# Optimization experiments

Measured on AMD Instinct MI355X. Metric: run time of the kernel, lower is better.

## Reference

```python
import jax, jax.numpy as jnp
import numpy as np

EPS = 1e-5
K = 20

def knn_idx(x, k):
    # x: (B, N, C) -> indices of k nearest neighbors (by negative squared distance, includes self)
    sq = jnp.sum(x * x, axis=-1)                                  # (B, N)
    d = 2.0 * jnp.einsum('bnc,bmc->bnm', x, x) - sq[:, :, None] - sq[:, None, :]
    return jax.lax.top_k(d, k)[1]                                 # (B, N, k)

def edge_conv(x, k, W, g, b, rm, rv):
    # x: (B, N, C); W: (O, 2C); BN params: (O,). Returns (B, N, O).
    idx = knn_idx(x, k)
    feat = jax.vmap(lambda xt, i: xt[i])(x, idx)                  # (B, N, k, C) neighbor gather
    ctr = jnp.broadcast_to(x[:, :, None, :], feat.shape)
    edge = jnp.concatenate([feat - ctr, ctr], axis=-1)            # (B, N, k, 2C)
    h = jnp.einsum('bnkc,oc->bnko', edge, W)                      # 1x1 conv
    h = g * (h - rm) * jax.lax.rsqrt(rv + EPS) + b                # BN (eval, running stats)
    h = jnp.where(h > 0, h, 0.2 * h)                              # LeakyReLU(0.2)
    return jnp.max(h, axis=2)                                     # max over k

def bn(h, g, b, rm, rv):
    return g * (h - rm) * jax.lax.rsqrt(rv + EPS) + b

def lrelu(h):
    return jnp.where(h > 0, h, 0.2 * h)

def _bn_params(key, c):
    k1, k2 = jax.random.split(key)
    g = 1.0 + 0.1 * jax.random.normal(k1, (c,), dtype=jnp.float32)
    b = 0.1 * jax.random.normal(k2, (c,), dtype=jnp.float32)
    return g, b, jnp.zeros((c,), jnp.float32), jnp.ones((c,), jnp.float32)

def setup_inputs() -> dict:
    key = jax.random.key(0)
    ks = jax.random.split(key, 16)
    B, Cin, N = 8, 6, 4096
    d = {'x': jax.random.normal(ks[0], (B, Cin, N), dtype=jnp.float32)}
    def w(k, o, i):
        return jax.random.normal(k, (o, i), dtype=jnp.float32) * (1.0 / np.sqrt(i))
    d['W1'] = w(ks[1], 64, 12);   d['g1'], d['b1'], d['m1'], d['v1'] = _bn_params(ks[2], 64)
    d['W2'] = w(ks[3], 64, 128);  d['g2'], d['b2'], d['m2'], d['v2'] = _bn_params(ks[4], 64)
    d['W3'] = w(ks[5], 128, 128); d['g3'], d['b3'], d['m3'], d['v3'] = _bn_params(ks[6], 128)
    d['W4'] = w(ks[7], 256, 256); d['g4'], d['b4'], d['m4'], d['v4'] = _bn_params(ks[8], 256)
    d['W5'] = w(ks[9], 1024, 512); d['g5'], d['b5'], d['m5'], d['v5'] = _bn_params(ks[10], 1024)
    d['L1'] = w(ks[11], 512, 2048); d['gl1'], d['bl1'], d['ml1'], d['vl1'] = _bn_params(ks[12], 512)
    d['L2'] = w(ks[13], 256, 512); d['L2b'] = jnp.zeros((256,), jnp.float32)
    d['gl2'], d['bl2'], d['ml2'], d['vl2'] = _bn_params(ks[14], 256)
    d['L3'] = w(ks[15], 2, 256);  d['L3b'] = jnp.zeros((2,), jnp.float32)
    return d

def reference(x, W1, g1, b1, m1, v1, W2, g2, b2, m2, v2, W3, g3, b3, m3, v3,
              W4, g4, b4, m4, v4, W5, g5, b5, m5, v5,
              L1, gl1, bl1, ml1, vl1, L2, L2b, gl2, bl2, ml2, vl2, L3, L3b):
    xt = jnp.transpose(x, (0, 2, 1))                              # (B, N, 6)
    x1 = edge_conv(xt, K, W1, g1, b1, m1, v1)                     # (B, N, 64)
    x2 = edge_conv(x1, K, W2, g2, b2, m2, v2)                     # (B, N, 64)
    x3 = edge_conv(x2, K, W3, g3, b3, m3, v3)                     # (B, N, 128)
    x4 = edge_conv(x3, K, W4, g4, b4, m4, v4)                     # (B, N, 256)
    xc = jnp.concatenate([x1, x2, x3, x4], axis=-1)               # (B, N, 512)
    h = lrelu(bn(jnp.einsum('bnc,oc->bno', xc, W5), g5, b5, m5, v5))  # (B, N, 1024)
    pooled = jnp.concatenate([jnp.max(h, axis=1), jnp.mean(h, axis=1)], axis=-1)  # (B, 2048)
    o = lrelu(bn(pooled @ L1.T, gl1, bl1, ml1, vl1))
    o = lrelu(bn(o @ L2.T + L2b, gl2, bl2, ml2, vl2))
    return o @ L3.T + L3b                                         # (B, 2)
```

## Files before the change

kernel.cpp:

```cpp
#include <hip/hip_runtime.h>


#define NPTS   4096
#define NB     8
#define BNR    32768
#define KNN    20
#define EPSBN  1e-5f
#define CAP    12

__device__ __forceinline__ float lrelu(float x){ return x > 0.f ? x : 0.2f*x; }

__global__ __launch_bounds__(256) void k_transpose_pad(const float* __restrict__ x,
                                                       float* __restrict__ xt){
  int id = blockIdx.x*256 + threadIdx.x;
  int b = id >> 12, n = id & (NPTS-1);
  const float* xb = x + (size_t)b*6*NPTS + n;
  float* o = xt + (size_t)id*8;
#pragma unroll
  for (int c = 0; c < 6; ++c) o[c] = xb[(size_t)c*NPTS];
  o[6] = 0.f; o[7] = 0.f;
}

__global__ __launch_bounds__(256) void k_sqnorm(const float* __restrict__ X, int xstride, int c4,
                                                float* __restrict__ sq){
  int id = blockIdx.x*256 + threadIdx.x;
  const float4* r = (const float4*)(X + (size_t)id*xstride);
  float s = 0.f;
  for (int c = 0; c < c4; ++c){ float4 v = r[c]; s += v.x*v.x + v.y*v.y + v.z*v.z + v.w*v.w; }
  sq[id] = s;
}

template<int K>
__global__ __launch_bounds__(256) void k_knn_fused(const float* __restrict__ X, int xstride,
                                                   const float* __restrict__ sqv,
                                                   int* __restrict__ idx){
  constexpr int BK = (K < 32) ? K : 32;
  __shared__ float As[BK][68];
  __shared__ float Bs[BK][132];
  __shared__ float sqs[128];
  __shared__ float thr[64];
  __shared__ float lv[64][KNN];
  __shared__ int   li[64][KNN];
  __shared__ int   cnt[64];
  __shared__ float cv[64][CAP];
  __shared__ int   ci[64][CAP];

  const int b  = blockIdx.y;
  const int i0 = blockIdx.x * 64;
  const int tid = threadIdx.x, tx = tid & 15, ty = tid >> 4;
  const float* Xb  = X + (size_t)b * NPTS * xstride;
  const float* sqb = sqv + b * NPTS;

  if (tid < 64){
    thr[tid] = -3e38f; cnt[tid] = 0;
#pragma unroll
    for (int j = 0; j < KNN; ++j){ lv[tid][j] = -3e38f; li[tid][j] = 0; }
  }
  float sqi[4];
#pragma unroll
  for (int r = 0; r < 4; ++r) sqi[r] = sqb[i0 + ty*4 + r];

  for (int j0 = 0; j0 < NPTS; j0 += 128){
    float acc[4][8] = {};
    for (int k0 = 0; k0 < K; k0 += BK){
      {
        int row = tid & 63, q = tid >> 6;
        const float* src = Xb + (size_t)(i0 + row)*xstride + k0;
#pragma unroll
        for (int k = q*(BK/4); k < (q+1)*(BK/4); ++k) As[k][row] = src[k];
      }
      {
        int col = tid & 127, h = tid >> 7;
        const float* src = Xb + (size_t)(j0 + col)*xstride + k0;
#pragma unroll
        for (int k = h*(BK/2); k < (h+1)*(BK/2); ++k) Bs[k][col] = src[k];
      }
      if (k0 == 0 && tid < 128) sqs[tid] = sqb[j0 + tid];
      __syncthreads();
#pragma unroll
      for (int kk = 0; kk < BK; ++kk){
        float a[4], bb_[8];
        *(float4*)a        = *(const float4*)&As[kk][ty*4];
        *(float4*)&bb_[0]  = *(const float4*)&Bs[kk][tx*4];
        *(float4*)&bb_[4]  = *(const float4*)&Bs[kk][64 + tx*4];
#pragma unroll
        for (int r = 0; r < 4; ++r)
#pragma unroll
          for (int c = 0; c < 8; ++c)
            acc[r][c] = fmaf(a[r], bb_[c], acc[r][c]);
      }
      __syncthreads();
    }
    float sq8[8];
#pragma unroll
    for (int c = 0; c < 4; ++c){ sq8[c] = sqs[tx*4 + c]; sq8[c+4] = sqs[64 + tx*4 + c]; }

    unsigned pending = 0xFFFFFFFFu;
    while (true){
      if (pending){
        float tr[4];
#pragma unroll
        for (int r = 0; r < 4; ++r) tr[r] = thr[ty*4 + r];
#pragma unroll
        for (int r = 0; r < 4; ++r)
#pragma unroll
          for (int c = 0; c < 8; ++c){
            unsigned bit = 1u << (r*8 + c);
            if (pending & bit){
              float val = 2.f*acc[r][c] - sqi[r] - sq8[c];
              if (val <= tr[r]) pending &= ~bit;
              else {
                int row = ty*4 + r;
                int pos = atomicAdd(&cnt[row], 1);
                if (pos < CAP){
                  int col = (c < 4) ? (j0 + tx*4 + c) : (j0 + 64 + tx*4 + c - 4);
                  cv[row][pos] = val; ci[row][pos] = col;
                  pending &= ~bit;
                }
              }
            }
          }
      }
      int any = __syncthreads_or(pending != 0u);
      if (tid < 64){
        int n = min(cnt[tid], CAP);
        for (int i2 = 0; i2 < n; ++i2){
          float val = cv[tid][i2]; int cc = ci[tid][i2];
          if (val > lv[tid][KNN-1]){
            int j = KNN-1;
            while (j > 0 && lv[tid][j-1] < val){
              lv[tid][j] = lv[tid][j-1]; li[tid][j] = li[tid][j-1]; --j;
            }
            lv[tid][j] = val; li[tid][j] = cc;
          }
        }
        thr[tid] = lv[tid][KNN-1];
        cnt[tid] = 0;
      }
      __syncthreads();
      if (!any) break;
    }
  }
  if (tid < 64){
    int gn = b*NPTS + i0 + tid;
#pragma unroll
    for (int j = 0; j < KNN; ++j) idx[(size_t)gn*KNN + j] = li[tid][j];
  }
}

__global__ __launch_bounds__(256) void k_gemm_pq(const float* __restrict__ X, int xstride, int Kdim,
                                                 const float* __restrict__ W, int wstride, int Och,
                                                 float* __restrict__ PQ){
  __shared__ float Xs[16][132];
  __shared__ float Ws[16][68];
  const int m0 = blockIdx.x*128, o0 = blockIdx.y*64;
  const int tid = threadIdx.x, tx = tid & 15, ty = tid >> 4;
  const int O2 = 2*Och;
  float acc[8][4] = {};
  for (int k0 = 0; k0 < Kdim; k0 += 16){
#pragma unroll
    for (int i = 0; i < 8; ++i){
      int li = tid + 256*i;
      int row = li >> 4, kk = li & 15;
      bool ok = (k0 + kk) < Kdim;
      Xs[kk][row] = ok ? X[(size_t)(m0+row)*xstride + k0+kk] : 0.f;
    }
#pragma unroll
    for (int i = 0; i < 4; ++i){
      int li = tid + 256*i;
      int row = li >> 4, kk = li & 15;
      int orow = o0 + row;
      const float* wr = (orow < Och) ? (W + (size_t)orow*wstride)
                                     : (W + (size_t)(orow-Och)*wstride + Kdim);
      bool ok = (k0 + kk) < Kdim;
      Ws[kk][row] = ok ? wr[k0+kk] : 0.f;
    }
    __syncthreads();
#pragma unroll
    for (int kk = 0; kk < 16; ++kk){
      float xa[8], wb[4];
      *(float4*)&xa[0] = *(const float4*)&Xs[kk][ty*8];
      *(float4*)&xa[4] = *(const float4*)&Xs[kk][ty*8+4];
      *(float4*)wb     = *(const float4*)&Ws[kk][tx*4];
#pragma unroll
      for (int i = 0; i < 8; ++i)
#pragma unroll
        for (int j = 0; j < 4; ++j)
          acc[i][j] = fmaf(xa[i], wb[j], acc[i][j]);
    }
    __syncthreads();
  }
#pragma unroll
  for (int i = 0; i < 8; ++i){
    float4 v = make_float4(acc[i][0], acc[i][1], acc[i][2], acc[i][3]);
    *(float4*)&PQ[(size_t)(m0+ty*8+i)*O2 + o0 + tx*4] = v;
  }
}

__global__ __launch_bounds__(256) void k_gather_conv(const float* __restrict__ PQ,
                                                     const int* __restrict__ idx,
                                                     const float* __restrict__ g,
                                                     const float* __restrict__ bb,
                                                     const float* __restrict__ rm,
                                                     const float* __restrict__ rv,
                                                     float* __restrict__ Out, int oshift, int choff){
  const int O = 1 << oshift;
  int id = blockIdx.x*256 + threadIdx.x;
  int gn = id >> oshift;
  int o  = id & (O-1);
  int bbase = (gn >> 12) * NPTS;
  const int* ip = idx + (size_t)gn*KNN;
  float vmax = -3e38f, vmin = 3e38f;
#pragma unroll
  for (int k = 0; k < KNN; ++k){
    int m = ip[k];
    float v = PQ[((size_t)(bbase + m) << (oshift+1)) + o];
    vmax = fmaxf(vmax, v);
    vmin = fminf(vmin, v);
  }
  float scale = g[o] * rsqrtf(rv[o] + EPSBN);
  float beta  = bb[o] - rm[o]*scale;
  float R = (scale >= 0.f) ? vmax : vmin;
  size_t self = (size_t)gn << (oshift+1);
  float h = R - PQ[self + o] + PQ[self + O + o];
  Out[(size_t)gn*512 + choff + o] = lrelu(fmaf(scale, h, beta));
}

__global__ __launch_bounds__(256) void k_gemm_w5_pool(const float* __restrict__ X,
                                                      const float* __restrict__ W,
                                                      const float* __restrict__ g,
                                                      const float* __restrict__ bb,
                                                      const float* __restrict__ rm,
                                                      const float* __restrict__ rv,
                                                      float* __restrict__ pmax,
                                                      float* __restrict__ psum){
  __shared__ float Xs[16][132];
  __shared__ float Ws[16][132];
  __shared__ float red[2][16][128];
  const int m0 = blockIdx.x*128, o0 = blockIdx.y*128;
  const int tid = threadIdx.x, tx = tid & 15, ty = tid >> 4;
  float acc[8][8] = {};
  for (int k0 = 0; k0 < 512; k0 += 16){
#pragma unroll
    for (int i = 0; i < 8; ++i){
      int li = tid + 256*i;
      int row = li >> 4, kk = li & 15;
      Xs[kk][row] = X[(size_t)(m0+row)*512 + k0+kk];
      Ws[kk][row] = W[(size_t)(o0+row)*512 + k0+kk];
    }
    __syncthreads();
#pragma unroll
    for (int kk = 0; kk < 16; ++kk){
      float xa[8], wb[8];
      *(float4*)&xa[0] = *(const float4*)&Xs[kk][ty*8];
      *(float4*)&xa[4] = *(const float4*)&Xs[kk][ty*8+4];
      *(float4*)&wb[0] = *(const float4*)&Ws[kk][tx*4];
      *(float4*)&wb[4] = *(const float4*)&Ws[kk][64 + tx*4];
#pragma unroll
      for (int i = 0; i < 8; ++i)
#pragma unroll
        for (int j = 0; j < 8; ++j)
          acc[i][j] = fmaf(xa[i], wb[j], acc[i][j]);
    }
    __syncthreads();
  }
#pragma unroll
  for (int j = 0; j < 8; ++j){
    int ocol = (j < 4) ? (tx*4 + j) : (64 + tx*4 + j - 4);
    int o = o0 + ocol;
    float scale = g[o] * rsqrtf(rv[o] + EPSBN);
    float beta  = bb[o] - rm[o]*scale;
    float mx = -3e38f, sm = 0.f;
#pragma unroll
    for (int i = 0; i < 8; ++i){
      float h = lrelu(fmaf(scale, acc[i][j], beta));
      mx = fmaxf(mx, h);
      sm += h;
    }
    red[0][ty][ocol] = mx;
    red[1][ty][ocol] = sm;
  }
  __syncthreads();
  if (tid < 128){
    float mx = -3e38f, sm = 0.f;
#pragma unroll
    for (int t = 0; t < 16; ++t){
      mx = fmaxf(mx, red[0][t][tid]);
      sm += red[1][t][tid];
    }
    pmax[(size_t)blockIdx.x*1024 + o0 + tid] = mx;
    psum[(size_t)blockIdx.x*1024 + o0 + tid] = sm;
  }
}

__global__ __launch_bounds__(256) void k_pool_reduce(const float* __restrict__ pmax,
                                                     const float* __restrict__ psum,
                                                     float* __restrict__ pooled){
  int id = blockIdx.x*256 + threadIdx.x;
  int b = id >> 10, o = id & 1023;
  float mx = -3e38f, sm = 0.f;
  for (int t = 0; t < 32; ++t){
    mx = fmaxf(mx, pmax[(size_t)(b*32+t)*1024 + o]);
    sm += psum[(size_t)(b*32+t)*1024 + o];
  }
  pooled[(size_t)b*2048 + o] = mx;
  pooled[(size_t)b*2048 + 1024 + o] = sm * (1.f/NPTS);
}

__global__ __launch_bounds__(256) void k_fc1(const float* __restrict__ pooled,
                                             const float* __restrict__ W,
                                             const float* __restrict__ g,
                                             const float* __restrict__ bb,
                                             const float* __restrict__ rm,
                                             const float* __restrict__ rv,
                                             float* __restrict__ out){
  __shared__ float4 xs[512];
  int b = blockIdx.x >> 1;
  int o = ((blockIdx.x & 1) << 8) + threadIdx.x;
  const float4* pr = (const float4*)(pooled + (size_t)b*2048);
  for (int l = threadIdx.x; l < 512; l += 256) xs[l] = pr[l];
  __syncthreads();
  const float4* wr = (const float4*)(W + (size_t)o*2048);
  float s0=0.f, s1=0.f, s2=0.f, s3=0.f;
#pragma unroll 4
  for (int c = 0; c < 512; ++c){
    float4 w = wr[c], v = xs[c];
    s0 = fmaf(v.x, w.x, s0); s1 = fmaf(v.y, w.y, s1);
    s2 = fmaf(v.z, w.z, s2); s3 = fmaf(v.w, w.w, s3);
  }
  float h = (s0+s1)+(s2+s3);
  float scale = g[o] * rsqrtf(rv[o] + EPSBN);
  float beta  = bb[o] - rm[o]*scale;
  out[(size_t)b*512 + o] = lrelu(fmaf(scale, h, beta));
}

__global__ __launch_bounds__(256) void k_fc2(const float* __restrict__ in,
                                             const float* __restrict__ W,
                                             const float* __restrict__ bias,
                                             const float* __restrict__ g,
                                             const float* __restrict__ bb,
                                             const float* __restrict__ rm,
                                             const float* __restrict__ rv,
                                             float* __restrict__ out){
  __shared__ float4 xs[128];
  int b = blockIdx.x;
  int o = threadIdx.x;
  const float4* pr = (const float4*)(in + (size_t)b*512);
  if (threadIdx.x < 128) xs[threadIdx.x] = pr[threadIdx.x];
  __syncthreads();
  const float4* wr = (const float4*)(W + (size_t)o*512);
  float s0=0.f, s1=0.f, s2=0.f, s3=0.f;
#pragma unroll 4
  for (int c = 0; c < 128; ++c){
    float4 w = wr[c], v = xs[c];
    s0 = fmaf(v.x, w.x, s0); s1 = fmaf(v.y, w.y, s1);
    s2 = fmaf(v.z, w.z, s2); s3 = fmaf(v.w, w.w, s3);
  }
  float h = (s0+s1)+(s2+s3) + bias[o];
  float scale = g[o] * rsqrtf(rv[o] + EPSBN);
  float beta  = bb[o] - rm[o]*scale;
  out[(size_t)b*256 + o] = lrelu(fmaf(scale, h, beta));
}

__global__ __launch_bounds__(64) void k_fc3(const float* __restrict__ in,
                                            const float* __restrict__ W,
                                            const float* __restrict__ bias,
                                            float* __restrict__ out){
  int t = threadIdx.x;
  if (t >= 16) return;
  int b = t >> 1, o = t & 1;
  const float* xr = in + (size_t)b*256;
  const float* wr = W + (size_t)o*256;
  float s = 0.f;
  for (int c = 0; c < 256; ++c) s = fmaf(xr[c], wr[c], s);
  out[b*2 + o] = s + bias[o];
}

extern "C" void kernel_launch(void* const* d_in, const int* in_sizes, int n_in,
                              void* d_out, int out_size, void* d_ws, size_t ws_size,
                              hipStream_t stream){
  (void)in_sizes; (void)n_in; (void)out_size;
  const float* x   = (const float*)d_in[0];
  const float* W1  = (const float*)d_in[1];
  const float* g1  = (const float*)d_in[2];
  const float* b1  = (const float*)d_in[3];
  const float* m1  = (const float*)d_in[4];
  const float* v1  = (const float*)d_in[5];
  const float* W2  = (const float*)d_in[6];
  const float* g2  = (const float*)d_in[7];
  const float* b2  = (const float*)d_in[8];
  const float* m2  = (const float*)d_in[9];
  const float* v2  = (const float*)d_in[10];
  const float* W3  = (const float*)d_in[11];
  const float* g3  = (const float*)d_in[12];
  const float* b3  = (const float*)d_in[13];
  const float* m3  = (const float*)d_in[14];
  const float* v3  = (const float*)d_in[15];
  const float* W4  = (const float*)d_in[16];
  const float* g4  = (const float*)d_in[17];
  const float* b4  = (const float*)d_in[18];
  const float* m4  = (const float*)d_in[19];
  const float* v4  = (const float*)d_in[20];
  const float* W5  = (const float*)d_in[21];
  const float* g5  = (const float*)d_in[22];
  const float* b5  = (const float*)d_in[23];
  const float* m5  = (const float*)d_in[24];
  const float* v5  = (const float*)d_in[25];
  const float* L1  = (const float*)d_in[26];
  const float* gl1 = (const float*)d_in[27];
  const float* bl1 = (const float*)d_in[28];
  const float* ml1 = (const float*)d_in[29];
  const float* vl1 = (const float*)d_in[30];
  const float* L2  = (const float*)d_in[31];
  const float* L2b = (const float*)d_in[32];
  const float* gl2 = (const float*)d_in[33];
  const float* bl2 = (const float*)d_in[34];
  const float* ml2 = (const float*)d_in[35];
  const float* vl2 = (const float*)d_in[36];
  const float* L3  = (const float*)d_in[37];
  const float* L3b = (const float*)d_in[38];

  float* ws   = (float*)d_ws;
  float* xt   = ws;
  float* sq   = ws + 262144;
  int*   idx  = (int*)(ws + 294912);
  float* PQ   = ws + 950272;
  float* xc   = ws + 17727488;
  float* pmax = ws + 34504704;
  float* psum = ws + 34766848;
  float* pool = ws + 35028992;
  float* oA   = ws + 35045376;
  float* oB   = ws + 35049472;
  if (ws_size < (size_t)35051520 * 4) return;

  k_transpose_pad<<<128, 256, 0, stream>>>(x, xt);

  k_sqnorm<<<128, 256, 0, stream>>>(xt, 8, 2, sq);
  k_knn_fused<8><<<dim3(64,8), 256, 0, stream>>>(xt, 8, sq, idx);
  k_gemm_pq<<<dim3(256,2), 256, 0, stream>>>(xt, 8, 6, W1, 12, 64, PQ);
  k_gather_conv<<<8192, 256, 0, stream>>>(PQ, idx, g1, b1, m1, v1, xc, 6, 0);

  k_sqnorm<<<128, 256, 0, stream>>>(xc, 512, 16, sq);
  k_knn_fused<64><<<dim3(64,8), 256, 0, stream>>>(xc, 512, sq, idx);
  k_gemm_pq<<<dim3(256,2), 256, 0, stream>>>(xc, 512, 64, W2, 128, 64, PQ);
  k_gather_conv<<<8192, 256, 0, stream>>>(PQ, idx, g2, b2, m2, v2, xc, 6, 64);

  k_sqnorm<<<128, 256, 0, stream>>>(xc + 64, 512, 16, sq);
  k_knn_fused<64><<<dim3(64,8), 256, 0, stream>>>(xc + 64, 512, sq, idx);
  k_gemm_pq<<<dim3(256,4), 256, 0, stream>>>(xc + 64, 512, 64, W3, 128, 128, PQ);
  k_gather_conv<<<16384, 256, 0, stream>>>(PQ, idx, g3, b3, m3, v3, xc, 7, 128);

  k_sqnorm<<<128, 256, 0, stream>>>(xc + 128, 512, 32, sq);
  k_knn_fused<128><<<dim3(64,8), 256, 0, stream>>>(xc + 128, 512, sq, idx);
  k_gemm_pq<<<dim3(256,8), 256, 0, stream>>>(xc + 128, 512, 128, W4, 256, 256, PQ);
  k_gather_conv<<<32768, 256, 0, stream>>>(PQ, idx, g4, b4, m4, v4, xc, 8, 256);

  k_gemm_w5_pool<<<dim3(256,8), 256, 0, stream>>>(xc, W5, g5, b5, m5, v5, pmax, psum);
  k_pool_reduce<<<32, 256, 0, stream>>>(pmax, psum, pool);

  k_fc1<<<16, 256, 0, stream>>>(pool, L1, gl1, bl1, ml1, vl1, oA);
  k_fc2<<<8, 256, 0, stream>>>(oA, L2, L2b, gl2, bl2, ml2, vl2, oB);
  k_fc3<<<1, 64, 0, stream>>>(oB, L3, L3b, (float*)d_out);
}
```

Before: 3.325 ms.

## Split KNN column range across blocks and merge partial top-k lists

The fused KNN kernel previously launched only 512 blocks (64×8), each scanning all 4096 candidate columns. It now splits the columns into four slices via a new grid dimension, writes per-slice top-20 candidates to a workspace buffer, and adds a merge kernel that runs a register-resident sorted insertion per point. The goal is to fill the GPU with four times as many blocks for the dominant KNN stage. The cost is an extra launch and extra global traffic for the candidate lists per layer. BK is also reduced to 16 and the shared arrays are padded to cut LDS use and bank conflicts.

```diff
diff --git a/kernel.cpp b/kernel.cpp
--- a/kernel.cpp
+++ b/kernel.cpp
@@ -7,8 +7,21 @@
 #define KNN    20
 #define EPSBN  1e-5f
 #define CAP    12
+#define NSPL   4
 
 __device__ __forceinline__ float lrelu(float x){ return x > 0.f ? x : 0.2f*x; }
+
+__device__ __forceinline__ void topk_insert(float (&bv)[KNN], int (&bi)[KNN], float d, int mi){
+#pragma unroll
+  for (int j = 0; j < KNN; ++j){
+    bool take = d > bv[j];
+    float nv = take ? d : bv[j];
+    int   ni = take ? mi : bi[j];
+    float od = take ? bv[j] : d;
+    int   oi = take ? bi[j] : mi;
+    bv[j] = nv; bi[j] = ni; d = od; mi = oi;
+  }
+}
 
 __global__ __launch_bounds__(256) void k_transpose_pad(const float* __restrict__ x,
                                                        float* __restrict__ xt){
@@ -33,20 +46,24 @@
 template<int K>
 __global__ __launch_bounds__(256) void k_knn_fused(const float* __restrict__ X, int xstride,
                                                    const float* __restrict__ sqv,
-                                                   int* __restrict__ idx){
-  constexpr int BK = (K < 32) ? K : 32;
+                                                   float* __restrict__ cand_v,
+                                                   int* __restrict__ cand_i){
+  constexpr int BK   = (K < 16) ? K : 16;
+  constexpr int COLS = NPTS / NSPL;
   __shared__ float As[BK][68];
   __shared__ float Bs[BK][132];
   __shared__ float sqs[128];
   __shared__ float thr[64];
-  __shared__ float lv[64][KNN];
-  __shared__ int   li[64][KNN];
+  __shared__ float lv[64][21];
+  __shared__ int   li[64][21];
   __shared__ int   cnt[64];
-  __shared__ float cv[64][CAP];
-  __shared__ int   ci[64][CAP];
-
-  const int b  = blockIdx.y;
+  __shared__ float cv[64][13];
+  __shared__ int   ci[64][13];
+
+  const int b  = blockIdx.z;
   const int i0 = blockIdx.x * 64;
+  const int sp = blockIdx.y;
+  const int c0 = sp * COLS;
   const int tid = threadIdx.x, tx = tid & 15, ty = tid >> 4;
   const float* Xb  = X + (size_t)b * NPTS * xstride;
   const float* sqb = sqv + b * NPTS;
@@ -60,7 +77,7 @@
 #pragma unroll
   for (int r = 0; r < 4; ++r) sqi[r] = sqb[i0 + ty*4 + r];
 
-  for (int j0 = 0; j0 < NPTS; j0 += 128){
+  for (int j0 = c0; j0 < c0 + COLS; j0 += 128){
     float acc[4][8] = {};
     for (int k0 = 0; k0 < K; k0 += BK){
       {
@@ -144,8 +161,30 @@
   if (tid < 64){
     int gn = b*NPTS + i0 + tid;
 #pragma unroll
-    for (int j = 0; j < KNN; ++j) idx[(size_t)gn*KNN + j] = li[tid][j];
-  }
+    for (int j = 0; j < KNN; ++j){
+      cand_v[(size_t)(sp*KNN + j)*BNR + gn] = lv[tid][j];
+      cand_i[(size_t)(sp*KNN + j)*BNR + gn] = li[tid][j];
+    }
+  }
+}
+
+__global__ __launch_bounds__(256) void k_knn_merge(const float* __restrict__ cand_v,
+                                                   const int* __restrict__ cand_i,
+                                                   int* __restrict__ idx){
+  int gn = blockIdx.x*256 + threadIdx.x;
+  float bv[KNN]; int bi[KNN];
+#pragma unroll
+  for (int j = 0; j < KNN; ++j){ bv[j] = -3e38f; bi[j] = -1; }
+  for (int s = 0; s < NSPL; ++s){
+#pragma unroll 1
+    for (int t = 0; t < KNN; ++t){
+      float d  = cand_v[(size_t)(s*KNN+t)*BNR + gn];
+      int   mi = cand_i[(size_t)(s*KNN+t)*BNR + gn];
+      if (d > bv[KNN-1]) topk_insert(bv, bi, d, mi);
+    }
+  }
+#pragma unroll
+  for (int j = 0; j < KNN; ++j) idx[(size_t)gn*KNN + j] = bi[j];
 }
 
 __global__ __launch_bounds__(256) void k_gemm_pq(const float* __restrict__ X, int xstride, int Kdim,
@@ -420,38 +459,44 @@
   const float* L3  = (const float*)d_in[37];
   const float* L3b = (const float*)d_in[38];
 
-  float* ws   = (float*)d_ws;
-  float* xt   = ws;
-  float* sq   = ws + 262144;
-  int*   idx  = (int*)(ws + 294912);
-  float* PQ   = ws + 950272;
-  float* xc   = ws + 17727488;
-  float* pmax = ws + 34504704;
-  float* psum = ws + 34766848;
-  float* pool = ws + 35028992;
-  float* oA   = ws + 35045376;
-  float* oB   = ws + 35049472;
-  if (ws_size < (size_t)35051520 * 4) return;
+  float* ws    = (float*)d_ws;
+  float* xt    = ws;
+  float* sq    = ws + 262144;
+  int*   idx   = (int*)(ws + 294912);
+  float* candv = ws + 950272;
+  int*   candi = (int*)(ws + 3571712);
+  float* PQ    = ws + 6193152;
+  float* xc    = ws + 22970368;
+  float* pmax  = ws + 39747584;
+  float* psum  = ws + 40009728;
+  float* pool  = ws + 40271872;
+  float* oA    = ws + 40288256;
+  float* oB    = ws + 40292352;
+  if (ws_size < (size_t)40294400 * 4) return;
 
   k_transpose_pad<<<128, 256, 0, stream>>>(x, xt);
 
   k_sqnorm<<<128, 256, 0, stream>>>(xt, 8, 2, sq);
-  k_knn_fused<8><<<dim3(64,8), 256, 0, stream>>>(xt, 8, sq, idx);
+  k_knn_fused<8><<<dim3(64,NSPL,8), 256, 0, stream>>>(xt, 8, sq, candv, candi);
+  k_knn_merge<<<128, 256, 0, stream>>>(candv, candi, idx);
   k_gemm_pq<<<dim3(256,2), 256, 0, stream>>>(xt, 8, 6, W1, 12, 64, PQ);
   k_gather_conv<<<8192, 256, 0, stream>>>(PQ, idx, g1, b1, m1, v1, xc, 6, 0);
 
   k_sqnorm<<<128, 256, 0, stream>>>(xc, 512, 16, sq);
-  k_knn_fused<64><<<dim3(64,8), 256, 0, stream>>>(xc, 512, sq, idx);
+  k_knn_fused<64><<<dim3(64,NSPL,8), 256, 0, stream>>>(xc, 512, sq, candv, candi);
+  k_knn_merge<<<128, 256, 0, stream>>>(candv, candi, idx);
   k_gemm_pq<<<dim3(256,2), 256, 0, stream>>>(xc, 512, 64, W2, 128, 64, PQ);
   k_gather_conv<<<8192, 256, 0, stream>>>(PQ, idx, g2, b2, m2, v2, xc, 6, 64);
 
   k_sqnorm<<<128, 256, 0, stream>>>(xc + 64, 512, 16, sq);
-  k_knn_fused<64><<<dim3(64,8), 256, 0, stream>>>(xc + 64, 512, sq, idx);
+  k_knn_fused<64><<<dim3(64,NSPL,8), 256, 0, stream>>>(xc + 64, 512, sq, candv, candi);
+  k_knn_merge<<<128, 256, 0, stream>>>(candv, candi, idx);
   k_gemm_pq<<<dim3(256,4), 256, 0, stream>>>(xc + 64, 512, 64, W3, 128, 128, PQ);
   k_gather_conv<<<16384, 256, 0, stream>>>(PQ, idx, g3, b3, m3, v3, xc, 7, 128);
 
   k_sqnorm<<<128, 256, 0, stream>>>(xc + 128, 512, 32, sq);
-  k_knn_fused<128><<<dim3(64,8), 256, 0, stream>>>(xc + 128, 512, sq, idx);
+  k_knn_fused<128><<<dim3(64,NSPL,8), 256, 0, stream>>>(xc + 128, 512, sq, candv, candi);
+  k_knn_merge<<<128, 256, 0, stream>>>(candv, candi, idx);
   k_gemm_pq<<<dim3(256,8), 256, 0, stream>>>(xc + 128, 512, 128, W4, 256, 256, PQ);
   k_gather_conv<<<32768, 256, 0, stream>>>(PQ, idx, g4, b4, m4, v4, xc, 8, 256);
 
```

Result: slower. 4.242 ms (+27.6%).
